# Kernel tuning notes

Measured on AMD Instinct MI355X. Metric: run time of the kernel, lower is better.

## Reference

```python
import jax, jax.numpy as jnp
import numpy as np

N_NODES = 100000
N_EDGES = 1600000
C_IN = 128
C_OUT = 128
BN_EPS = 1e-5
LEAKY_SLOPE = 0.01


def setup_inputs() -> dict:
    key = jax.random.key(0)
    k1, k2, k3 = jax.random.split(key, 3)
    x = jax.random.normal(k1, (N_NODES, C_IN), dtype=jnp.float32)
    edge_index = jax.random.randint(k2, (2, N_EDGES), 0, N_NODES, dtype=jnp.int64)
    # GCNConv linear weight (glorot-ish scale) and bias
    W = jax.random.normal(k3, (C_IN, C_OUT), dtype=jnp.float32) * (1.0 / np.sqrt(C_IN))
    bias = jnp.zeros((C_OUT,), dtype=jnp.float32)
    # BatchNorm affine params
    gamma = jnp.ones((C_OUT,), dtype=jnp.float32)
    beta = jnp.zeros((C_OUT,), dtype=jnp.float32)
    return {"x": x, "edge_index": edge_index, "W": W, "bias": bias,
            "gamma": gamma, "beta": beta}


def reference(x, edge_index, W, bias, gamma, beta):
    N = x.shape[0]
    # --- GCNConv (add self loops, symmetric degree normalization) ---
    loop = jnp.arange(N, dtype=edge_index.dtype)
    src = jnp.concatenate([edge_index[0], loop])  # message sources (x_j)
    dst = jnp.concatenate([edge_index[1], loop])  # aggregation targets
    ones = jnp.ones(src.shape[0], dtype=x.dtype)
    deg = jax.ops.segment_sum(ones, dst, num_segments=N)
    dinv_sqrt = jnp.where(deg > 0, jax.lax.rsqrt(deg), 0.0).astype(x.dtype)
    norm = dinv_sqrt[src] * dinv_sqrt[dst]  # [E+N]

    h = x @ W                                # [N, C_out], transform first
    msg = h[src] * norm[:, None]             # gather + edge weighting
    out = jax.ops.segment_sum(msg, dst, num_segments=N) + bias  # scatter-add

    # --- LeakyReLU ---
    out = jax.nn.leaky_relu(out, negative_slope=LEAKY_SLOPE)

    # --- BatchNorm over nodes (training-mode batch stats, biased var) ---
    mean = out.mean(axis=0)
    var = out.var(axis=0)
    out = (out - mean) * jax.lax.rsqrt(var + BN_EPS) * gamma + beta
    return out
```

## Files before the change

kernel.cpp:

```cpp
#include <hip/hip_runtime.h>

#define N_NODES 100000
#define N_EDGES 1600000
#define C 128
#define LEAKY 0.01f
#define BN_EPS 1e-5f
#define NB_C 391
#define PB 391
#define PBLK 4096
#define STASH 8192
#define NBG 1563
#define NAGG 6250
#define NRED 64

typedef __attribute__((ext_vector_type(8))) short short8;
typedef __attribute__((ext_vector_type(4))) float f32x4;

__device__ __forceinline__ unsigned short f2bf(float f) {
    unsigned int u = __builtin_bit_cast(unsigned int, f);
    u += 0x7FFFu + ((u >> 16) & 1u);
    return (unsigned short)(u >> 16);
}
__device__ __forceinline__ float bf2f(unsigned short b) {
    unsigned int u = ((unsigned int)b) << 16;
    return __builtin_bit_cast(float, u);
}

__global__ __launch_bounds__(256) void k_coarse(const int* __restrict__ dst,
                                                int* __restrict__ blk_cnt,
                                                const float* __restrict__ W,
                                                unsigned short* __restrict__ wt,
                                                unsigned short* __restrict__ hs) {
    __shared__ int lh[NB_C];
    int tid = threadIdx.x, blk = blockIdx.x;
    int gi = blk * 256 + tid;
    if (gi < C * C) wt[gi] = f2bf(W[(gi & 127) * C + (gi >> 7)]);
    if (gi < C) hs[(size_t)N_NODES * C + gi] = 0;
    for (int i = tid; i < NB_C; i += 256) lh[i] = 0;
    __syncthreads();
    #pragma unroll
    for (int it = 0; it < PBLK / 256; ++it) {
        int e = blk * PBLK + it * 256 + tid;
        if (e < N_EDGES) atomicAdd(&lh[dst[e] >> 8], 1);
    }
    __syncthreads();
    for (int i = tid; i < NB_C; i += 256) blk_cnt[i * PB + blk] = lh[i];
}

__global__ __launch_bounds__(512) void k_offsets(const int* __restrict__ blk_cnt,
                                                 int* __restrict__ offset,
                                                 int* __restrict__ total) {
    __shared__ int tmp[512];
    int t = threadIdx.x, k = blockIdx.x;
    int v = (t < PB) ? blk_cnt[k * PB + t] : 0;
    tmp[t] = v;
    __syncthreads();
    for (int off = 1; off < 512; off <<= 1) {
        int u = (t >= off) ? tmp[t - off] : 0;
        __syncthreads();
        tmp[t] += u;
        __syncthreads();
    }
    if (t < PB) offset[k * PB + t] = tmp[t] - v;
    if (t == 511) total[k] = tmp[511];
}

__global__ __launch_bounds__(512) void k_cbase(const int* __restrict__ total,
                                               int* __restrict__ cbase,
                                               int* __restrict__ offs) {
    __shared__ int tmp[512];
    int t = threadIdx.x;
    int v = (t < NB_C) ? total[t] : 0;
    tmp[t] = v;
    __syncthreads();
    for (int off = 1; off < 512; off <<= 1) {
        int u = (t >= off) ? tmp[t - off] : 0;
        __syncthreads();
        tmp[t] += u;
        __syncthreads();
    }
    if (t < NB_C) cbase[t] = tmp[t] - v;
    if (t == 0) { cbase[NB_C] = N_EDGES; offs[N_NODES] = N_EDGES; }
}

__global__ __launch_bounds__(256) void k_partition(const int* __restrict__ src,
                                                   const int* __restrict__ dst,
                                                   const int* __restrict__ cbase,
                                                   const int* __restrict__ offset,
                                                   unsigned int* __restrict__ pairs) {
    __shared__ int lh[NB_C];
    __shared__ int lbase[NB_C];
    int tid = threadIdx.x, blk = blockIdx.x;
    for (int i = tid; i < NB_C; i += 256) {
        lh[i] = 0;
        lbase[i] = cbase[i] + offset[i * PB + blk];
    }
    __syncthreads();
    #pragma unroll
    for (int it = 0; it < PBLK / 256; ++it) {
        int e = blk * PBLK + it * 256 + tid;
        if (e < N_EDGES) {
            int d = dst[e];
            int b = d >> 8;
            int r = atomicAdd(&lh[b], 1);
            pairs[lbase[b] + r] = (unsigned int)src[e] | ((unsigned int)(d & 255) << 17);
        }
    }
}

__global__ __launch_bounds__(256) void k_fine(const unsigned int* __restrict__ pairs,
                                              const int* __restrict__ cbase,
                                              float* __restrict__ dinv,
                                              int* __restrict__ offs,
                                              int* __restrict__ srt) {
    __shared__ int hist[256];
    __shared__ int loff[256];
    __shared__ int cnt2[256];
    __shared__ unsigned int stash[STASH];
    int tid = threadIdx.x, blk = blockIdx.x;
    int nbase = blk * 256;
    int nn = (nbase + 256 <= N_NODES) ? 256 : (N_NODES - nbase);
    int ebeg = cbase[blk];
    int ne = cbase[blk + 1] - ebeg;

    hist[tid] = 0; cnt2[tid] = 0;
    __syncthreads();
    for (int k = tid; k < ne; k += 256) {
        unsigned int pk = pairs[ebeg + k];
        if (k < STASH) stash[k] = pk;
        atomicAdd(&hist[pk >> 17], 1);
    }
    __syncthreads();
    if (tid < nn) dinv[nbase + tid] = rsqrtf((float)(hist[tid] + 1));
    loff[tid] = hist[tid];
    __syncthreads();
    for (int off = 1; off < 256; off <<= 1) {
        int u = (tid >= off) ? loff[tid - off] : 0;
        __syncthreads();
        loff[tid] += u;
        __syncthreads();
    }
    loff[tid] -= hist[tid];
    if (tid < nn) offs[nbase + tid] = ebeg + loff[tid];
    __syncthreads();
    for (int k = tid; k < ne; k += 256) {
        unsigned int pk = (k < STASH) ? stash[k] : pairs[ebeg + k];
        int dl = pk >> 17;
        int r = atomicAdd(&cnt2[dl], 1);
        srt[ebeg + loff[dl] + r] = (int)(pk & 0x1FFFFu);
    }
}

__global__ __launch_bounds__(256) void k_gemm_hs(const float* __restrict__ x,
                                                 const unsigned short* __restrict__ wt,
                                                 const float* __restrict__ dinv,
                                                 unsigned short* __restrict__ hs) {
    int tile = blockIdx.x * 4 + (threadIdx.x >> 6);
    if (tile >= N_NODES / 16) return;
    int lane = threadIdx.x & 63;
    int row0 = tile * 16;
    int ar = lane & 15;
    int kg = (lane >> 4) * 8;

    short8 a[4];
    #pragma unroll
    for (int kk = 0; kk < 4; ++kk) {
        const float* p = &x[(size_t)(row0 + ar) * C + kk * 32 + kg];
        float4 p0 = *(const float4*)p;
        float4 p1 = *(const float4*)(p + 4);
        short8 av;
        av[0] = (short)f2bf(p0.x); av[1] = (short)f2bf(p0.y);
        av[2] = (short)f2bf(p0.z); av[3] = (short)f2bf(p0.w);
        av[4] = (short)f2bf(p1.x); av[5] = (short)f2bf(p1.y);
        av[6] = (short)f2bf(p1.z); av[7] = (short)f2bf(p1.w);
        a[kk] = av;
    }

    int rb = (lane >> 4) * 4;
    float dv[4];
    #pragma unroll
    for (int r = 0; r < 4; ++r) dv[r] = dinv[row0 + rb + r];

    #pragma unroll
    for (int ct = 0; ct < 8; ++ct) {
        f32x4 acc = {0.f, 0.f, 0.f, 0.f};
        #pragma unroll
        for (int kk = 0; kk < 4; ++kk) {
            short8 b = *(const short8*)&wt[(size_t)(ct * 16 + ar) * C + kk * 32 + kg];
            acc = __builtin_amdgcn_mfma_f32_16x16x32_bf16(a[kk], b, acc, 0, 0, 0);
        }
        int col = ct * 16 + ar;
        #pragma unroll
        for (int r = 0; r < 4; ++r)
            hs[(size_t)(row0 + rb + r) * C + col] = f2bf(acc[r] * dv[r]);
    }
}

__global__ __launch_bounds__(256) void k_aggregate(const unsigned int* __restrict__ hs32,
                                                   const int* __restrict__ srt,
                                                   const int* __restrict__ offs,
                                                   const float* __restrict__ dinv,
                                                   const float* __restrict__ bias,
                                                   unsigned int* __restrict__ vb32,
                                                   float* __restrict__ part) {
    __shared__ float red_s[4][C];
    __shared__ float red_q[4][C];
    int wave = threadIdx.x >> 6, lane = threadIdx.x & 63;
    float2 bb = ((const float2*)bias)[lane];
    float s0 = 0.f, s1 = 0.f, q0 = 0.f, q1 = 0.f;

    #pragma unroll
    for (int g = 0; g < 4; ++g) {
        int node = __builtin_amdgcn_readfirstlane(blockIdx.x * 16 + g * 4 + wave);
        float dn = dinv[node];
        int beg = offs[node];
        int end = offs[node + 1];

        unsigned int ms = hs32[(size_t)node * 64 + lane];
        float ax0 = __builtin_bit_cast(float, ms << 16);
        float ax1 = __builtin_bit_cast(float, ms & 0xFFFF0000u);

        for (int k = beg; k < end; k += 8) {
            int idx[8];
            #pragma unroll
            for (int i = 0; i < 8; ++i) {
                int ki = k + i;
                idx[i] = (ki < end) ? srt[ki] : N_NODES;
            }
            unsigned int m[8];
            #pragma unroll
            for (int i = 0; i < 8; ++i) m[i] = hs32[(size_t)idx[i] * 64 + lane];
            #pragma unroll
            for (int i = 0; i < 8; ++i) {
                ax0 += __builtin_bit_cast(float, m[i] << 16);
                ax1 += __builtin_bit_cast(float, m[i] & 0xFFFF0000u);
            }
        }

        float v0 = dn * ax0 + bb.x; v0 = v0 > 0.f ? v0 : LEAKY * v0;
        float v1 = dn * ax1 + bb.y; v1 = v1 > 0.f ? v1 : LEAKY * v1;
        vb32[(size_t)node * 64 + lane] =
            (unsigned int)f2bf(v0) | ((unsigned int)f2bf(v1) << 16);
        s0 += v0; q0 += v0 * v0;
        s1 += v1; q1 += v1 * v1;
    }

    red_s[wave][lane * 2] = s0;  red_s[wave][lane * 2 + 1] = s1;
    red_q[wave][lane * 2] = q0;  red_q[wave][lane * 2 + 1] = q1;
    __syncthreads();
    int tid = threadIdx.x;
    if (tid < C) {
        part[(size_t)blockIdx.x * 256 + tid] =
            red_s[0][tid] + red_s[1][tid] + red_s[2][tid] + red_s[3][tid];
    } else {
        int c = tid - C;
        part[(size_t)blockIdx.x * 256 + tid] =
            red_q[0][c] + red_q[1][c] + red_q[2][c] + red_q[3][c];
    }
}

__global__ __launch_bounds__(256) void k_reduce(const float* __restrict__ part,
                                                float* __restrict__ part2) {
    int t = threadIdx.x, b = blockIdx.x;
    float s = 0.0f;
    for (int r = b; r < NAGG; r += NRED) s += part[(size_t)r * 256 + t];
    part2[(size_t)b * 256 + t] = s;
}

__global__ __launch_bounds__(256) void k_params(const float* __restrict__ part2,
                                                const float* __restrict__ gamma,
                                                const float* __restrict__ beta,
                                                float* __restrict__ scale,
                                                float* __restrict__ shift) {
    __shared__ float tot[256];
    int t = threadIdx.x;
    float s = 0.0f;
    #pragma unroll
    for (int b = 0; b < NRED; ++b) s += part2[(size_t)b * 256 + t];
    tot[t] = s;
    __syncthreads();
    if (t < C) {
        float inv_n = 1.0f / (float)N_NODES;
        float mean = tot[t] * inv_n;
        float var = tot[C + t] * inv_n - mean * mean;
        float sc = gamma[t] * rsqrtf(var + BN_EPS);
        scale[t] = sc;
        shift[t] = beta[t] - mean * sc;
    }
}

__global__ __launch_bounds__(256) void k_apply(const short8* __restrict__ vb8,
                                               const float* __restrict__ scale,
                                               const float* __restrict__ shift,
                                               float* __restrict__ out) {
    int i = blockIdx.x * 256 + threadIdx.x;
    int c8 = i & 15;
    short8 v = vb8[i];
    float4 sc0 = *(const float4*)&scale[c8 * 8];
    float4 sc1 = *(const float4*)&scale[c8 * 8 + 4];
    float4 sh0 = *(const float4*)&shift[c8 * 8];
    float4 sh1 = *(const float4*)&shift[c8 * 8 + 4];
    float4 o0, o1;
    o0.x = bf2f((unsigned short)v[0]) * sc0.x + sh0.x;
    o0.y = bf2f((unsigned short)v[1]) * sc0.y + sh0.y;
    o0.z = bf2f((unsigned short)v[2]) * sc0.z + sh0.z;
    o0.w = bf2f((unsigned short)v[3]) * sc0.w + sh0.w;
    o1.x = bf2f((unsigned short)v[4]) * sc1.x + sh1.x;
    o1.y = bf2f((unsigned short)v[5]) * sc1.y + sh1.y;
    o1.z = bf2f((unsigned short)v[6]) * sc1.z + sh1.z;
    o1.w = bf2f((unsigned short)v[7]) * sc1.w + sh1.w;
    float4* op = (float4*)out + (size_t)i * 2;
    op[0] = o0;
    op[1] = o1;
}

extern "C" void kernel_launch(void* const* d_in, const int* in_sizes, int n_in,
                              void* d_out, int out_size, void* d_ws, size_t ws_size,
                              hipStream_t stream) {
    const float* x     = (const float*)d_in[0];
    const int*   edge  = (const int*)d_in[1];
    const float* W     = (const float*)d_in[2];
    const float* bias  = (const float*)d_in[3];
    const float* gamma = (const float*)d_in[4];
    const float* beta  = (const float*)d_in[5];
    float* out = (float*)d_out;
    char* ws = (char*)d_ws;

    unsigned short* hs    = (unsigned short*)ws;  ws += (size_t)(N_NODES + 1) * C * 2;
    unsigned short* vb    = (unsigned short*)ws;  ws += (size_t)N_NODES * C * 2;
    unsigned short* wt    = (unsigned short*)ws;  ws += (size_t)C * C * 2;
    unsigned int*   pairs = (unsigned int*)ws;    ws += (size_t)N_EDGES * 4;
    int*   srt     = (int*)ws;                    ws += (size_t)N_EDGES * 4;
    int*   blk_cnt = (int*)ws;                    ws += (size_t)NB_C * PB * 4;
    int*   offset  = (int*)ws;                    ws += (size_t)NB_C * PB * 4;
    int*   total   = (int*)ws;                    ws += 512 * 4;
    int*   cbase   = (int*)ws;                    ws += 512 * 4;
    int*   offs    = (int*)ws;                    ws += (size_t)(N_NODES + 1) * 4;
    float* dinv    = (float*)ws;                  ws += (size_t)N_NODES * 4;
    float* part2   = (float*)ws;                  ws += (size_t)NRED * 256 * 4;
    float* scale   = (float*)ws;                  ws += C * 4;
    float* shift   = (float*)ws;

    float* part = (float*)pairs;

    const int* src = edge;
    const int* dst = edge + N_EDGES;

    k_coarse   <<<PB,                    256, 0, stream>>>(dst, blk_cnt, W, wt, hs);
    k_offsets  <<<NB_C,                  512, 0, stream>>>(blk_cnt, offset, total);
    k_cbase    <<<1,                     512, 0, stream>>>(total, cbase, offs);
    k_partition<<<PB,                    256, 0, stream>>>(src, dst, cbase, offset, pairs);
    k_fine     <<<NB_C,                  256, 0, stream>>>(pairs, cbase, dinv, offs, srt);
    k_gemm_hs  <<<NBG,                   256, 0, stream>>>(x, wt, dinv, hs);
    k_aggregate<<<NAGG,                  256, 0, stream>>>((const unsigned int*)hs, srt, offs, dinv, bias,
                                                           (unsigned int*)vb, part);
    k_reduce   <<<NRED,                  256, 0, stream>>>(part, part2);
    k_params   <<<1,                     256, 0, stream>>>(part2, gamma, beta, scale, shift);
    k_apply    <<<N_NODES * C / 8 / 256, 256, 0, stream>>>((const short8*)vb, scale, shift, out);
}
```

Before: 189.5 us.

## Merge single-block finalize kernels via last-block tickets and stage GEMM input in LDS

The single-block cbase scan and BN-params kernels are folded into their producer kernels using an atomic ticket, so the last block to finish does the final step. This removes two kernel launches and their dependency gaps. Separately, the GEMM kernel now loads a 64-row x tile into shared memory with coalesced float4 loads before building the MFMA operands. The risks are the extra threadfence/atomic cost, and the extra LDS use, which may lower occupancy.

After: 242.8 us. +28.1%, slower.

```diff
diff --git a/kernel.cpp b/kernel.cpp
--- a/kernel.cpp
+++ b/kernel.cpp
@@ -30,12 +30,14 @@
                                                 int* __restrict__ blk_cnt,
                                                 const float* __restrict__ W,
                                                 unsigned short* __restrict__ wt,
-                                                unsigned short* __restrict__ hs) {
+                                                unsigned short* __restrict__ hs,
+                                                int* __restrict__ tickets) {
     __shared__ int lh[NB_C];
     int tid = threadIdx.x, blk = blockIdx.x;
     int gi = blk * 256 + tid;
     if (gi < C * C) wt[gi] = f2bf(W[(gi & 127) * C + (gi >> 7)]);
     if (gi < C) hs[(size_t)N_NODES * C + gi] = 0;
+    if (gi < 2) tickets[gi] = 0;
     for (int i = tid; i < NB_C; i += 256) lh[i] = 0;
     __syncthreads();
     #pragma unroll
@@ -49,8 +51,12 @@
 
 __global__ __launch_bounds__(512) void k_offsets(const int* __restrict__ blk_cnt,
                                                  int* __restrict__ offset,
-                                                 int* __restrict__ total) {
+                                                 int* __restrict__ total,
+                                                 int* __restrict__ cbase,
+                                                 int* __restrict__ offs,
+                                                 int* __restrict__ ticket) {
     __shared__ int tmp[512];
+    __shared__ int amLast;
     int t = threadIdx.x, k = blockIdx.x;
     int v = (t < PB) ? blk_cnt[k * PB + t] : 0;
     tmp[t] = v;
@@ -63,15 +69,15 @@
     }
     if (t < PB) offset[k * PB + t] = tmp[t] - v;
     if (t == 511) total[k] = tmp[511];
-}
-
-__global__ __launch_bounds__(512) void k_cbase(const int* __restrict__ total,
-                                               int* __restrict__ cbase,
-                                               int* __restrict__ offs) {
-    __shared__ int tmp[512];
-    int t = threadIdx.x;
-    int v = (t < NB_C) ? total[t] : 0;
-    tmp[t] = v;
+
+    __threadfence();
+    if (t == 0) amLast = (atomicAdd(ticket, 1) == NB_C - 1);
+    __syncthreads();
+    if (!amLast) return;
+    __threadfence();
+
+    int v2 = (t < NB_C) ? total[t] : 0;
+    tmp[t] = v2;
     __syncthreads();
     for (int off = 1; off < 512; off <<= 1) {
         int u = (t >= off) ? tmp[t - off] : 0;
@@ -79,7 +85,7 @@
         tmp[t] += u;
         __syncthreads();
     }
-    if (t < NB_C) cbase[t] = tmp[t] - v;
+    if (t < NB_C) cbase[t] = tmp[t] - v2;
     if (t == 0) { cbase[NB_C] = N_EDGES; offs[N_NODES] = N_EDGES; }
 }
 
@@ -155,19 +161,35 @@
                                                  const unsigned short* __restrict__ wt,
                                                  const float* __restrict__ dinv,
                                                  unsigned short* __restrict__ hs) {
-    int tile = blockIdx.x * 4 + (threadIdx.x >> 6);
+    __shared__ float xs[64 * 132];
+    int tid = threadIdx.x;
+    int row0g = blockIdx.x * 64;
+
+    #pragma unroll
+    for (int it = 0; it < 8; ++it) {
+        int q = it * 256 + tid;
+        int r = q >> 5, c4 = q & 31;
+        int gr = row0g + r;
+        float4 v = (gr < N_NODES) ? ((const float4*)x)[(size_t)gr * 32 + c4]
+                                  : make_float4(0.f, 0.f, 0.f, 0.f);
+        *(float4*)&xs[r * 132 + c4 * 4] = v;
+    }
+    __syncthreads();
+
+    int wid = tid >> 6;
+    int tile = blockIdx.x * 4 + wid;
     if (tile >= N_NODES / 16) return;
-    int lane = threadIdx.x & 63;
+    int lane = tid & 63;
     int row0 = tile * 16;
     int ar = lane & 15;
     int kg = (lane >> 4) * 8;
+    int lrow = wid * 16 + ar;
 
     short8 a[4];
     #pragma unroll
     for (int kk = 0; kk < 4; ++kk) {
-        const float* p = &x[(size_t)(row0 + ar) * C + kk * 32 + kg];
-        float4 p0 = *(const float4*)p;
-        float4 p1 = *(const float4*)(p + 4);
+        float4 p0 = *(const float4*)&xs[lrow * 132 + kk * 32 + kg];
+        float4 p1 = *(const float4*)&xs[lrow * 132 + kk * 32 + kg + 4];
         short8 av;
         av[0] = (short)f2bf(p0.x); av[1] = (short)f2bf(p0.y);
         av[2] = (short)f2bf(p0.z); av[3] = (short)f2bf(p0.w);
@@ -260,24 +282,29 @@
 }
 
 __global__ __launch_bounds__(256) void k_reduce(const float* __restrict__ part,
-                                                float* __restrict__ part2) {
+                                                float* __restrict__ part2,
+                                                const float* __restrict__ gamma,
+                                                const float* __restrict__ beta,
+                                                float* __restrict__ scale,
+                                                float* __restrict__ shift,
+                                                int* __restrict__ ticket) {
+    __shared__ int amLast;
+    __shared__ float tot[256];
     int t = threadIdx.x, b = blockIdx.x;
     float s = 0.0f;
     for (int r = b; r < NAGG; r += NRED) s += part[(size_t)r * 256 + t];
     part2[(size_t)b * 256 + t] = s;
-}
-
-__global__ __launch_bounds__(256) void k_params(const float* __restrict__ part2,
-                                                const float* __restrict__ gamma,
-                                                const float* __restrict__ beta,
-                                                float* __restrict__ scale,
-                                                float* __restrict__ shift) {
-    __shared__ float tot[256];
-    int t = threadIdx.x;
-    float s = 0.0f;
-    #pragma unroll
-    for (int b = 0; b < NRED; ++b) s += part2[(size_t)b * 256 + t];
-    tot[t] = s;
+
+    __threadfence();
+    if (t == 0) amLast = (atomicAdd(ticket, 1) == NRED - 1);
+    __syncthreads();
+    if (!amLast) return;
+    __threadfence();
+
+    float ss = 0.0f;
+    #pragma unroll
+    for (int bb = 0; bb < NRED; ++bb) ss += part2[(size_t)bb * 256 + t];
+    tot[t] = ss;
     __syncthreads();
     if (t < C) {
         float inv_n = 1.0f / (float)N_NODES;
@@ -339,22 +366,21 @@
     float* dinv    = (float*)ws;                  ws += (size_t)N_NODES * 4;
     float* part2   = (float*)ws;                  ws += (size_t)NRED * 256 * 4;
     float* scale   = (float*)ws;                  ws += C * 4;
-    float* shift   = (float*)ws;
+    float* shift   = (float*)ws;                  ws += C * 4;
+    int*   tickets = (int*)ws;                    ws += 2 * 4;
 
     float* part = (float*)pairs;
 
     const int* src = edge;
     const int* dst = edge + N_EDGES;
 
-    k_coarse   <<<PB,                    256, 0, stream>>>(dst, blk_cnt, W, wt, hs);
-    k_offsets  <<<NB_C,                  512, 0, stream>>>(blk_cnt, offset, total);
-    k_cbase    <<<1,                     512, 0, stream>>>(total, cbase, offs);
+    k_coarse   <<<PB,                    256, 0, stream>>>(dst, blk_cnt, W, wt, hs, tickets);
+    k_offsets  <<<NB_C,                  512, 0, stream>>>(blk_cnt, offset, total, cbase, offs, &tickets[0]);
     k_partition<<<PB,                    256, 0, stream>>>(src, dst, cbase, offset, pairs);
     k_fine     <<<NB_C,                  256, 0, stream>>>(pairs, cbase, dinv, offs, srt);
     k_gemm_hs  <<<NBG,                   256, 0, stream>>>(x, wt, dinv, hs);
     k_aggregate<<<NAGG,                  256, 0, stream>>>((const unsigned int*)hs, srt, offs, dinv, bias,
                                                            (unsigned int*)vb, part);
-    k_reduce   <<<NRED,                  256, 0, stream>>>(part, part2);
-    k_params   <<<1,                     256, 0, stream>>>(part2, gamma, beta, scale, shift);
+    k_reduce   <<<NRED,                  256, 0, stream>>>(part, part2, gamma, beta, scale, shift, &tickets[1]);
     k_apply    <<<N_NODES * C / 8 / 256, 256, 0, stream>>>((const short8*)vb, scale, shift, out);
 }
```

## Split bf16 feature table into two 64-channel halves and aggregate each separately

Applied to the files above, without the earlier changes.

The GEMM now writes the transformed features into two separate 64-channel planes, and aggregation runs in two passes, one per plane. The intent is to halve the working set of the random gather so each plane (about 12.8 MB) fits better in L2/LLC and gets more cache hits. The cost is reading the edge list and offsets twice and launching an extra kernel. Each lane now does 2-byte gathers instead of 4-byte, so each gathered row is only 128 bytes.

Result: slower. 219.4 us (+15.8%).

```diff
diff --git a/kernel.cpp b/kernel.cpp
--- a/kernel.cpp
+++ b/kernel.cpp
@@ -30,12 +30,16 @@
                                                 int* __restrict__ blk_cnt,
                                                 const float* __restrict__ W,
                                                 unsigned short* __restrict__ wt,
-                                                unsigned short* __restrict__ hs) {
+                                                unsigned short* __restrict__ hsL,
+                                                unsigned short* __restrict__ hsH) {
     __shared__ int lh[NB_C];
     int tid = threadIdx.x, blk = blockIdx.x;
     int gi = blk * 256 + tid;
     if (gi < C * C) wt[gi] = f2bf(W[(gi & 127) * C + (gi >> 7)]);
-    if (gi < C) hs[(size_t)N_NODES * C + gi] = 0;
+    if (gi < 64) {
+        hsL[(size_t)N_NODES * 64 + gi] = 0;
+        hsH[(size_t)N_NODES * 64 + gi] = 0;
+    }
     for (int i = tid; i < NB_C; i += 256) lh[i] = 0;
     __syncthreads();
     #pragma unroll
@@ -154,7 +158,8 @@
 __global__ __launch_bounds__(256) void k_gemm_hs(const float* __restrict__ x,
                                                  const unsigned short* __restrict__ wt,
                                                  const float* __restrict__ dinv,
-                                                 unsigned short* __restrict__ hs) {
+                                                 unsigned short* __restrict__ hsL,
+                                                 unsigned short* __restrict__ hsH) {
     int tile = blockIdx.x * 4 + (threadIdx.x >> 6);
     if (tile >= N_NODES / 16) return;
     int lane = threadIdx.x & 63;
@@ -190,24 +195,27 @@
             acc = __builtin_amdgcn_mfma_f32_16x16x32_bf16(a[kk], b, acc, 0, 0, 0);
         }
         int col = ct * 16 + ar;
+        unsigned short* pl = (col < 64) ? hsL : hsH;
+        int c64 = col & 63;
         #pragma unroll
         for (int r = 0; r < 4; ++r)
-            hs[(size_t)(row0 + rb + r) * C + col] = f2bf(acc[r] * dv[r]);
-    }
-}
-
-__global__ __launch_bounds__(256) void k_aggregate(const unsigned int* __restrict__ hs32,
-                                                   const int* __restrict__ srt,
-                                                   const int* __restrict__ offs,
-                                                   const float* __restrict__ dinv,
-                                                   const float* __restrict__ bias,
-                                                   unsigned int* __restrict__ vb32,
-                                                   float* __restrict__ part) {
-    __shared__ float red_s[4][C];
-    __shared__ float red_q[4][C];
+            pl[(size_t)(row0 + rb + r) * 64 + c64] = f2bf(acc[r] * dv[r]);
+    }
+}
+
+__global__ __launch_bounds__(256) void k_aggregate_h(const unsigned short* __restrict__ pl,
+                                                     const int* __restrict__ srt,
+                                                     const int* __restrict__ offs,
+                                                     const float* __restrict__ dinv,
+                                                     const float* __restrict__ bias,
+                                                     unsigned short* __restrict__ vb,
+                                                     float* __restrict__ part,
+                                                     int chbase) {
+    __shared__ float red_s[4][64];
+    __shared__ float red_q[4][64];
     int wave = threadIdx.x >> 6, lane = threadIdx.x & 63;
-    float2 bb = ((const float2*)bias)[lane];
-    float s0 = 0.f, s1 = 0.f, q0 = 0.f, q1 = 0.f;
+    float bb = bias[chbase + lane];
+    float s = 0.f, q = 0.f;
 
     #pragma unroll
     for (int g = 0; g < 4; ++g) {
@@ -216,9 +224,7 @@
         int beg = offs[node];
         int end = offs[node + 1];
 
-        unsigned int ms = hs32[(size_t)node * 64 + lane];
-        float ax0 = __builtin_bit_cast(float, ms << 16);
-        float ax1 = __builtin_bit_cast(float, ms & 0xFFFF0000u);
+        float ax = bf2f(pl[(size_t)node * 64 + lane]);
 
         for (int k = beg; k < end; k += 8) {
             int idx[8];
@@ -227,35 +233,30 @@
                 int ki = k + i;
                 idx[i] = (ki < end) ? srt[ki] : N_NODES;
             }
-            unsigned int m[8];
+            unsigned short m[8];
             #pragma unroll
-            for (int i = 0; i < 8; ++i) m[i] = hs32[(size_t)idx[i] * 64 + lane];
+            for (int i = 0; i < 8; ++i) m[i] = pl[(size_t)idx[i] * 64 + lane];
             #pragma unroll
-            for (int i = 0; i < 8; ++i) {
-                ax0 += __builtin_bit_cast(float, m[i] << 16);
-                ax1 += __builtin_bit_cast(float, m[i] & 0xFFFF0000u);
-            }
+            for (int i = 0; i < 8; ++i) ax += bf2f(m[i]);
         }
 
-        float v0 = dn * ax0 + bb.x; v0 = v0 > 0.f ? v0 : LEAKY * v0;
-        float v1 = dn * ax1 + bb.y; v1 = v1 > 0.f ? v1 : LEAKY * v1;
-        vb32[(size_t)node * 64 + lane] =
-            (unsigned int)f2bf(v0) | ((unsigned int)f2bf(v1) << 16);
-        s0 += v0; q0 += v0 * v0;
-        s1 += v1; q1 += v1 * v1;
-    }
-
-    red_s[wave][lane * 2] = s0;  red_s[wave][lane * 2 + 1] = s1;
-    red_q[wave][lane * 2] = q0;  red_q[wave][lane * 2 + 1] = q1;
+        float v = dn * ax + bb;
+        v = v > 0.f ? v : LEAKY * v;
+        vb[(size_t)node * C + chbase + lane] = f2bf(v);
+        s += v; q += v * v;
+    }
+
+    red_s[wave][lane] = s;
+    red_q[wave][lane] = q;
     __syncthreads();
     int tid = threadIdx.x;
-    if (tid < C) {
-        part[(size_t)blockIdx.x * 256 + tid] =
+    if (tid < 64) {
+        part[(size_t)blockIdx.x * 256 + chbase + tid] =
             red_s[0][tid] + red_s[1][tid] + red_s[2][tid] + red_s[3][tid];
-    } else {
-        int c = tid - C;
-        part[(size_t)blockIdx.x * 256 + tid] =
-            red_q[0][c] + red_q[1][c] + red_q[2][c] + red_q[3][c];
+    } else if (tid < 128) {
+        int c2 = tid - 64;
+        part[(size_t)blockIdx.x * 256 + 128 + chbase + c2] =
+            red_q[0][c2] + red_q[1][c2] + red_q[2][c2] + red_q[3][c2];
     }
 }
 
@@ -326,7 +327,8 @@
     float* out = (float*)d_out;
     char* ws = (char*)d_ws;
 
-    unsigned short* hs    = (unsigned short*)ws;  ws += (size_t)(N_NODES + 1) * C * 2;
+    unsigned short* hsL   = (unsigned short*)ws;  ws += (size_t)(N_NODES + 1) * 64 * 2;
+    unsigned short* hsH   = (unsigned short*)ws;  ws += (size_t)(N_NODES + 1) * 64 * 2;
     unsigned short* vb    = (unsigned short*)ws;  ws += (size_t)N_NODES * C * 2;
     unsigned short* wt    = (unsigned short*)ws;  ws += (size_t)C * C * 2;
     unsigned int*   pairs = (unsigned int*)ws;    ws += (size_t)N_EDGES * 4;
@@ -346,15 +348,15 @@
     const int* src = edge;
     const int* dst = edge + N_EDGES;
 
-    k_coarse   <<<PB,                    256, 0, stream>>>(dst, blk_cnt, W, wt, hs);
-    k_offsets  <<<NB_C,                  512, 0, stream>>>(blk_cnt, offset, total);
-    k_cbase    <<<1,                     512, 0, stream>>>(total, cbase, offs);
-    k_partition<<<PB,                    256, 0, stream>>>(src, dst, cbase, offset, pairs);
-    k_fine     <<<NB_C,                  256, 0, stream>>>(pairs, cbase, dinv, offs, srt);
-    k_gemm_hs  <<<NBG,                   256, 0, stream>>>(x, wt, dinv, hs);
-    k_aggregate<<<NAGG,                  256, 0, stream>>>((const unsigned int*)hs, srt, offs, dinv, bias,
-                                                           (unsigned int*)vb, part);
-    k_reduce   <<<NRED,                  256, 0, stream>>>(part, part2);
-    k_params   <<<1,                     256, 0, stream>>>(part2, gamma, beta, scale, shift);
-    k_apply    <<<N_NODES * C / 8 / 256, 256, 0, stream>>>((const short8*)vb, scale, shift, out);
-}
+    k_coarse     <<<PB,                    256, 0, stream>>>(dst, blk_cnt, W, wt, hsL, hsH);
+    k_offsets    <<<NB_C,                  512, 0, stream>>>(blk_cnt, offset, total);
+    k_cbase      <<<1,                     512, 0, stream>>>(total, cbase, offs);
+    k_partition  <<<PB,                    256, 0, stream>>>(src, dst, cbase, offset, pairs);
+    k_fine       <<<NB_C,                  256, 0, stream>>>(pairs, cbase, dinv, offs, srt);
+    k_gemm_hs    <<<NBG,                   256, 0, stream>>>(x, wt, dinv, hsL, hsH);
+    k_aggregate_h<<<NAGG,                  256, 0, stream>>>(hsL, srt, offs, dinv, bias, vb, part, 0);
+    k_aggregate_h<<<NAGG,                  256, 0, stream>>>(hsH, srt, offs, dinv, bias, vb, part, 64);
+    k_reduce     <<<NRED,                  256, 0, stream>>>(part, part2);
+    k_params     <<<1,                     256, 0, stream>>>(part2, gamma, beta, scale, shift);
+    k_apply      <<<N_NODES * C / 8 / 256, 256, 0, stream>>>((const short8*)vb, scale, shift, out);
+}
```
